# Optimization experiments

Measured on AMD Instinct MI355X. Metric: run time of the kernel, lower is better.

The kernel has to match this reference:

```python
import jax, jax.numpy as jnp
import numpy as np

N_EMBD = 384
HEAD_SIZE = 64
BLOCK_SIZE = 64
SCALE = HEAD_SIZE * N_EMBD ** (-0.5)  # non-standard scale from source: k.shape[-1] * C**-0.5


def setup_inputs() -> dict:
    key = jax.random.key(0)
    kx, kk, kq, kv = jax.random.split(key, 4)
    B, T = 2048, BLOCK_SIZE
    x = jax.random.normal(kx, (B, T, N_EMBD), dtype=jnp.float32)
    # torch Linear(n_embd, head_size, bias=False): weight shape [head_size, n_embd], y = x @ W.T
    s = N_EMBD ** -0.5
    Wk = jax.random.uniform(kk, (HEAD_SIZE, N_EMBD), jnp.float32, -s, s)
    Wq = jax.random.uniform(kq, (HEAD_SIZE, N_EMBD), jnp.float32, -s, s)
    Wv = jax.random.uniform(kv, (HEAD_SIZE, N_EMBD), jnp.float32, -s, s)
    return {"x": x, "Wk": Wk, "Wq": Wq, "Wv": Wv}


def reference(x, Wk, Wq, Wv) -> jnp.ndarray:
    B, T, C = x.shape
    k = jnp.einsum("btc,hc->bth", x, Wk)  # [B,T,H]
    q = jnp.einsum("btc,hc->bth", x, Wq)
    v = jnp.einsum("btc,hc->bth", x, Wv)
    wei = jnp.einsum("bth,bsh->bts", q, k) * SCALE  # [B,T,T]
    causal = jnp.tril(jnp.ones((T, T), dtype=bool))
    wei = jnp.where(causal, wei, -jnp.inf)
    wei = jax.nn.softmax(wei, axis=-1)
    out = jnp.einsum("bts,bsh->bth", wei, v)  # [B,T,H]
    return out
```

## Files before the change

### kernel.cpp

```cpp
#include <hip/hip_runtime.h>

typedef _Float16 f16;
typedef _Float16 f16x8 __attribute__((ext_vector_type(8)));
typedef _Float16 f16x4 __attribute__((ext_vector_type(4)));
typedef float    f32x4 __attribute__((ext_vector_type(4)));

#define MFMA16(a, b, c) __builtin_amdgcn_mfma_f32_16x16x32_f16((a), (b), (c), 0, 0, 0)

constexpr int T = 64;
constexpr int C = 384;
constexpr int H = 64;
constexpr float SCALE = 3.26598632371090f;

__device__ __forceinline__ void load_lds16(const float* g, float* l) {
  __builtin_amdgcn_global_load_lds(
      (const __attribute__((address_space(1))) void*)g,
      (__attribute__((address_space(3))) void*)l, 16, 0, 0);
}

__global__ void pack_w(const float* __restrict__ Wk, const float* __restrict__ Wq,
                       const float* __restrict__ Wv, f16* __restrict__ Wp) {
  int tid = blockIdx.x * blockDim.x + threadIdx.x;
  if (tid >= 3 * 12 * 4 * 64) return;
  int lane = tid & 63;
  int tile = tid >> 6;
  int ht = tile & 3;
  int kt = (tile >> 2) % 12;
  int wi = tile / 48;
  const float* W = (wi == 0) ? Wk : ((wi == 1) ? Wq : Wv);
  int h = 16 * ht + (lane & 15);
  int c = 32 * kt + 8 * (lane >> 4);
  const float* src = W + h * C + c;
  f16x8 v;
#pragma unroll
  for (int j = 0; j < 8; ++j) v[j] = (f16)src[j];
  int tile2 = kt * 12 + wi * 4 + ht;
  *(f16x8*)(Wp + (size_t)tile2 * 512 + lane * 8) = v;
}

__global__ __launch_bounds__(256, 4) void proj_kqv(
    const float* __restrict__ x, const f16* __restrict__ Wp,
    f16* __restrict__ kg, f16* __restrict__ qg, f16* __restrict__ vtg) {
  __shared__ float xc[2][2048];

  const int b = blockIdx.x;
  const int tid = threadIdx.x;
  const int w = tid >> 6;
  const int lane = tid & 63;
  const int l15 = lane & 15;
  const int g = lane >> 4;

  const f32x4 vzero = {0.0f, 0.0f, 0.0f, 0.0f};
  f32x4 acc[3][4];
#pragma unroll
  for (int c = 0; c < 3; ++c)
#pragma unroll
    for (int tt = 0; tt < 4; ++tt) acc[c][tt] = vzero;

  const f16* wp_base[3];
  bool isV[3];
#pragma unroll
  for (int c = 0; c < 3; ++c) {
    int combo = 3 * w + c;
    wp_base[c] = Wp + (size_t)combo * 512 + lane * 8;
    isV[c] = (combo >= 8);
  }

  const float* xbase = x + (size_t)b * T * C;
  const float* gsrc = xbase + (size_t)(16 * w + l15) * C + g * 8;

  load_lds16(gsrc + 0, &xc[0][(2 * w + 0) * 256]);
  load_lds16(gsrc + 4, &xc[0][(2 * w + 1) * 256]);
  f16x8 wpc[3], wpn[3];
#pragma unroll
  for (int c = 0; c < 3; ++c) wpc[c] = *(const f16x8*)(wp_base[c]);
  asm volatile("s_waitcnt vmcnt(0)" ::: "memory");
  __builtin_amdgcn_s_barrier();

#pragma unroll
  for (int kt = 0; kt < 12; ++kt) {
    const int cur = kt & 1;
    if (kt + 1 < 12) {
      load_lds16(gsrc + (kt + 1) * 32 + 0, &xc[cur ^ 1][(2 * w + 0) * 256]);
      load_lds16(gsrc + (kt + 1) * 32 + 4, &xc[cur ^ 1][(2 * w + 1) * 256]);
#pragma unroll
      for (int c = 0; c < 3; ++c)
        wpn[c] = *(const f16x8*)(wp_base[c] + (size_t)(kt + 1) * 6144);
    }

    f16x8 xf[4];
#pragma unroll
    for (int tt = 0; tt < 4; ++tt) {
      f32x4 A0 = *(const f32x4*)&xc[cur][(2 * tt + 0) * 256 + lane * 4];
      f32x4 A1 = *(const f32x4*)&xc[cur][(2 * tt + 1) * 256 + lane * 4];
#pragma unroll
      for (int j = 0; j < 4; ++j) { xf[tt][j] = (f16)A0[j]; xf[tt][4 + j] = (f16)A1[j]; }
    }
#pragma unroll
    for (int c = 0; c < 3; ++c) {
      f16x8 wf = wpc[c];
      if (!isV[c]) {
#pragma unroll
        for (int tt = 0; tt < 4; ++tt) acc[c][tt] = MFMA16(wf, xf[tt], acc[c][tt]);
      } else {
#pragma unroll
        for (int tt = 0; tt < 4; ++tt) acc[c][tt] = MFMA16(xf[tt], wf, acc[c][tt]);
      }
      wpc[c] = wpn[c];
    }
    asm volatile("s_waitcnt vmcnt(0)" ::: "memory");
    __builtin_amdgcn_s_barrier();
  }

  f16* vt_lds = (f16*)&xc[0][0];
#pragma unroll
  for (int c = 0; c < 3; ++c) {
    int combo = 3 * w + c;
    int m = combo >> 2;
    int ht = combo & 3;
#pragma unroll
    for (int tt = 0; tt < 4; ++tt) {
      f16x4 pd;
#pragma unroll
      for (int r = 0; r < 4; ++r) pd[r] = (f16)acc[c][tt][r];
      if (m == 0) {
        *(f16x4*)(kg + ((size_t)b * 64 + 16 * tt + l15) * 64 + 16 * ht + 4 * g) = pd;
      } else if (m == 1) {
        *(f16x4*)(qg + ((size_t)b * 64 + 16 * tt + l15) * 64 + 16 * ht + 4 * g) = pd;
      } else {
        *(f16x4*)&vt_lds[(16 * ht + l15) * 68 + 16 * tt + 4 * g] = pd;
      }
    }
  }
  __syncthreads();
#pragma unroll
  for (int r = 0; r < 2; ++r) {
    int idx = tid + r * 256;
    f16x8 vv = *(const f16x8*)&vt_lds[(idx >> 3) * 68 + (idx & 7) * 8];
    *(f16x8*)(vtg + (size_t)b * 4096 + idx * 8) = vv;
  }
}

__global__ __launch_bounds__(256, 5) void attn64(
    const f16* __restrict__ kg, const f16* __restrict__ qg,
    const f16* __restrict__ vtg, float* __restrict__ out) {
  __shared__ f16 qp_lds[64][72];
  __shared__ f16 k_lds[64][72];
  __shared__ f16 vT_lds[64][72];

  const int b = blockIdx.x;
  const int tid = threadIdx.x;
  const int w = tid >> 6;
  const int lane = tid & 63;
  const int l15 = lane & 15;
  const int g = lane >> 4;
  const int t_ = 16 * w + l15;

  const size_t tb = (size_t)b * 4096;
  const int i0 = tid, i1 = tid + 256;
  f16x8 ka = *(const f16x8*)(kg + tb + (size_t)i0 * 8);
  f16x8 kb = *(const f16x8*)(kg + tb + (size_t)i1 * 8);
  f16x8 qa = *(const f16x8*)(qg + tb + (size_t)i0 * 8);
  f16x8 qb = *(const f16x8*)(qg + tb + (size_t)i1 * 8);
  f16x8 va = *(const f16x8*)(vtg + tb + (size_t)i0 * 8);
  f16x8 vb = *(const f16x8*)(vtg + tb + (size_t)i1 * 8);
  *(f16x8*)&k_lds[i0 >> 3][(i0 & 7) * 8] = ka;
  *(f16x8*)&k_lds[i1 >> 3][(i1 & 7) * 8] = kb;
  *(f16x8*)&qp_lds[i0 >> 3][(i0 & 7) * 8] = qa;
  *(f16x8*)&qp_lds[i1 >> 3][(i1 & 7) * 8] = qb;
  *(f16x8*)&vT_lds[i0 >> 3][(i0 & 7) * 8] = va;
  *(f16x8*)&vT_lds[i1 >> 3][(i1 & 7) * 8] = vb;
  __syncthreads();

  const f32x4 vzero = {0.0f, 0.0f, 0.0f, 0.0f};

  f32x4 accs[4];
#pragma unroll
  for (int i = 0; i < 4; ++i) accs[i] = vzero;
#pragma unroll
  for (int kt = 0; kt < 2; ++kt) {
    f16x8 qf = *(const f16x8*)&qp_lds[t_][32 * kt + 8 * g];
#pragma unroll
    for (int mt = 0; mt < 4; ++mt) {
      f16x8 kf = *(const f16x8*)&k_lds[16 * mt + l15][32 * kt + 8 * g];
      accs[mt] = MFMA16(kf, qf, accs[mt]);
    }
  }

  float e[16];
  float mx = -__builtin_inff();
#pragma unroll
  for (int mt = 0; mt < 4; ++mt) {
#pragma unroll
    for (int r = 0; r < 4; ++r) {
      int s = 16 * mt + 4 * g + r;
      float lv = accs[mt][r] * SCALE;
      lv = (s <= t_) ? lv : -__builtin_inff();
      e[mt * 4 + r] = lv;
      mx = fmaxf(mx, lv);
    }
  }
  mx = fmaxf(mx, __shfl_xor(mx, 16));
  mx = fmaxf(mx, __shfl_xor(mx, 32));
  float sm = 0.0f;
#pragma unroll
  for (int i = 0; i < 16; ++i) { e[i] = __expf(e[i] - mx); sm += e[i]; }
  sm += __shfl_xor(sm, 16);
  sm += __shfl_xor(sm, 32);
  const float inv = 1.0f / sm;
#pragma unroll
  for (int mt = 0; mt < 4; ++mt) {
    f16x4 pp;
#pragma unroll
    for (int r = 0; r < 4; ++r) pp[r] = (f16)(e[mt * 4 + r] * inv);
    *(f16x4*)&qp_lds[t_][16 * mt + 4 * g] = pp;
  }

  f32x4 acco[4];
#pragma unroll
  for (int i = 0; i < 4; ++i) acco[i] = vzero;
#pragma unroll
  for (int kt = 0; kt < 2; ++kt) {
    f16x8 pf = *(const f16x8*)&qp_lds[t_][32 * kt + 8 * g];
#pragma unroll
    for (int mt = 0; mt < 4; ++mt) {
      f16x8 vf = *(const f16x8*)&vT_lds[16 * mt + l15][32 * kt + 8 * g];
      acco[mt] = MFMA16(vf, pf, acco[mt]);
    }
  }

  float* orow = out + ((size_t)b * T + t_) * H;
#pragma unroll
  for (int mt = 0; mt < 4; ++mt) {
    *(f32x4*)(orow + 16 * mt + 4 * g) = acco[mt];
  }
}

extern "C" void kernel_launch(void* const* d_in, const int* in_sizes, int n_in,
                              void* d_out, int out_size, void* d_ws, size_t ws_size,
                              hipStream_t stream) {
  const float* x  = (const float*)d_in[0];
  const float* Wk = (const float*)d_in[1];
  const float* Wq = (const float*)d_in[2];
  const float* Wv = (const float*)d_in[3];
  float* out = (float*)d_out;

  f16* Wp  = (f16*)d_ws;
  f16* kg  = (f16*)((char*)d_ws + (1 << 18));
  f16* qg  = kg + (size_t)2048 * 64 * 64;
  f16* vtg = qg + (size_t)2048 * 64 * 64;

  pack_w<<<36, 256, 0, stream>>>(Wk, Wq, Wv, Wp);
  proj_kqv<<<2048, 256, 0, stream>>>(x, Wp, kg, qg, vtg);
  attn64<<<2048, 256, 0, stream>>>(kg, qg, vtg, out);
}
```

Measured before the change: 354.4 us.

## Restructure projection so each wave owns a row tile and streams x through registers

Each wave now computes all 12 output column blocks (K, Q, V) for its own 16 rows of x, so the x tile can be loaded straight into registers with a 4-deep prefetch ring. This drops the LDS staging and the per-k-step barriers. In exchange, every wave loads all 12 weight fragments per k step, which raises L2/global weight traffic and register pressure. Launch bounds are lowered to 2 blocks per SIMD to make room for the extra registers.

```diff
diff --git a/kernel.cpp b/kernel.cpp
--- a/kernel.cpp
+++ b/kernel.cpp
@@ -11,12 +11,6 @@
 constexpr int C = 384;
 constexpr int H = 64;
 constexpr float SCALE = 3.26598632371090f;
-
-__device__ __forceinline__ void load_lds16(const float* g, float* l) {
-  __builtin_amdgcn_global_load_lds(
-      (const __attribute__((address_space(1))) void*)g,
-      (__attribute__((address_space(3))) void*)l, 16, 0, 0);
-}
 
 __global__ void pack_w(const float* __restrict__ Wk, const float* __restrict__ Wq,
                        const float* __restrict__ Wv, f16* __restrict__ Wp) {
@@ -38,10 +32,10 @@
   *(f16x8*)(Wp + (size_t)tile2 * 512 + lane * 8) = v;
 }
 
-__global__ __launch_bounds__(256, 4) void proj_kqv(
+__global__ __launch_bounds__(256, 2) void proj_reg(
     const float* __restrict__ x, const f16* __restrict__ Wp,
     f16* __restrict__ kg, f16* __restrict__ qg, f16* __restrict__ vtg) {
-  __shared__ float xc[2][2048];
+  __shared__ f16 vt_lds[64][68];
 
   const int b = blockIdx.x;
   const int tid = threadIdx.x;
@@ -51,92 +45,78 @@
   const int g = lane >> 4;
 
   const f32x4 vzero = {0.0f, 0.0f, 0.0f, 0.0f};
-  f32x4 acc[3][4];
-#pragma unroll
-  for (int c = 0; c < 3; ++c)
-#pragma unroll
-    for (int tt = 0; tt < 4; ++tt) acc[c][tt] = vzero;
-
-  const f16* wp_base[3];
-  bool isV[3];
-#pragma unroll
-  for (int c = 0; c < 3; ++c) {
-    int combo = 3 * w + c;
-    wp_base[c] = Wp + (size_t)combo * 512 + lane * 8;
-    isV[c] = (combo >= 8);
-  }
-
-  const float* xbase = x + (size_t)b * T * C;
-  const float* gsrc = xbase + (size_t)(16 * w + l15) * C + g * 8;
-
-  load_lds16(gsrc + 0, &xc[0][(2 * w + 0) * 256]);
-  load_lds16(gsrc + 4, &xc[0][(2 * w + 1) * 256]);
-  f16x8 wpc[3], wpn[3];
-#pragma unroll
-  for (int c = 0; c < 3; ++c) wpc[c] = *(const f16x8*)(wp_base[c]);
-  asm volatile("s_waitcnt vmcnt(0)" ::: "memory");
-  __builtin_amdgcn_s_barrier();
+  f32x4 acc[12];
+#pragma unroll
+  for (int cb = 0; cb < 12; ++cb) acc[cb] = vzero;
+
+  const float* gsrc = x + (size_t)b * T * C + (size_t)(16 * w + l15) * C + 8 * g;
+  const f16* wsrc = Wp + lane * 8;
+
+  f32x4 xa[4], xb[4];
+#pragma unroll
+  for (int i = 0; i < 4; ++i) {
+    xa[i] = *(const f32x4*)(gsrc + i * 32 + 0);
+    xb[i] = *(const f32x4*)(gsrc + i * 32 + 4);
+  }
+  f16x8 wpc[12], wpn[12];
+#pragma unroll
+  for (int cb = 0; cb < 12; ++cb)
+    wpc[cb] = *(const f16x8*)(wsrc + (size_t)cb * 512);
 
 #pragma unroll
   for (int kt = 0; kt < 12; ++kt) {
-    const int cur = kt & 1;
+    const int sl = kt & 3;
+    f16x8 xf;
+    {
+      f32x4 A0 = xa[sl], A1 = xb[sl];
+#pragma unroll
+      for (int j = 0; j < 4; ++j) { xf[j] = (f16)A0[j]; xf[4 + j] = (f16)A1[j]; }
+    }
+    if (kt + 4 < 12) {
+      xa[sl] = *(const f32x4*)(gsrc + (kt + 4) * 32 + 0);
+      xb[sl] = *(const f32x4*)(gsrc + (kt + 4) * 32 + 4);
+    }
     if (kt + 1 < 12) {
-      load_lds16(gsrc + (kt + 1) * 32 + 0, &xc[cur ^ 1][(2 * w + 0) * 256]);
-      load_lds16(gsrc + (kt + 1) * 32 + 4, &xc[cur ^ 1][(2 * w + 1) * 256]);
-#pragma unroll
-      for (int c = 0; c < 3; ++c)
-        wpn[c] = *(const f16x8*)(wp_base[c] + (size_t)(kt + 1) * 6144);
-    }
-
-    f16x8 xf[4];
-#pragma unroll
-    for (int tt = 0; tt < 4; ++tt) {
-      f32x4 A0 = *(const f32x4*)&xc[cur][(2 * tt + 0) * 256 + lane * 4];
-      f32x4 A1 = *(const f32x4*)&xc[cur][(2 * tt + 1) * 256 + lane * 4];
-#pragma unroll
-      for (int j = 0; j < 4; ++j) { xf[tt][j] = (f16)A0[j]; xf[tt][4 + j] = (f16)A1[j]; }
-    }
-#pragma unroll
-    for (int c = 0; c < 3; ++c) {
-      f16x8 wf = wpc[c];
-      if (!isV[c]) {
-#pragma unroll
-        for (int tt = 0; tt < 4; ++tt) acc[c][tt] = MFMA16(wf, xf[tt], acc[c][tt]);
-      } else {
-#pragma unroll
-        for (int tt = 0; tt < 4; ++tt) acc[c][tt] = MFMA16(xf[tt], wf, acc[c][tt]);
-      }
-      wpc[c] = wpn[c];
-    }
-    asm volatile("s_waitcnt vmcnt(0)" ::: "memory");
-    __builtin_amdgcn_s_barrier();
-  }
-
-  f16* vt_lds = (f16*)&xc[0][0];
-#pragma unroll
-  for (int c = 0; c < 3; ++c) {
-    int combo = 3 * w + c;
-    int m = combo >> 2;
-    int ht = combo & 3;
-#pragma unroll
-    for (int tt = 0; tt < 4; ++tt) {
-      f16x4 pd;
-#pragma unroll
-      for (int r = 0; r < 4; ++r) pd[r] = (f16)acc[c][tt][r];
-      if (m == 0) {
-        *(f16x4*)(kg + ((size_t)b * 64 + 16 * tt + l15) * 64 + 16 * ht + 4 * g) = pd;
-      } else if (m == 1) {
-        *(f16x4*)(qg + ((size_t)b * 64 + 16 * tt + l15) * 64 + 16 * ht + 4 * g) = pd;
-      } else {
-        *(f16x4*)&vt_lds[(16 * ht + l15) * 68 + 16 * tt + 4 * g] = pd;
-      }
-    }
+#pragma unroll
+      for (int cb = 0; cb < 12; ++cb)
+        wpn[cb] = *(const f16x8*)(wsrc + ((size_t)(kt + 1) * 12 + cb) * 512);
+    }
+#pragma unroll
+    for (int cb = 0; cb < 8; ++cb)
+      acc[cb] = MFMA16(wpc[cb], xf, acc[cb]);
+#pragma unroll
+    for (int cb = 8; cb < 12; ++cb)
+      acc[cb] = MFMA16(xf, wpc[cb], acc[cb]);
+#pragma unroll
+    for (int cb = 0; cb < 12; ++cb) wpc[cb] = wpn[cb];
+  }
+
+#pragma unroll
+  for (int ht = 0; ht < 4; ++ht) {
+    f16x4 pd;
+#pragma unroll
+    for (int r = 0; r < 4; ++r) pd[r] = (f16)acc[0 + ht][r];
+    *(f16x4*)(kg + ((size_t)b * 64 + 16 * w + l15) * 64 + 16 * ht + 4 * g) = pd;
+  }
+#pragma unroll
+  for (int ht = 0; ht < 4; ++ht) {
+    f16x4 pd;
+#pragma unroll
+    for (int r = 0; r < 4; ++r) pd[r] = (f16)acc[4 + ht][r];
+    *(f16x4*)(qg + ((size_t)b * 64 + 16 * w + l15) * 64 + 16 * ht + 4 * g) = pd;
+  }
+#pragma unroll
+  for (int ht = 0; ht < 4; ++ht) {
+    f16x4 pd;
+#pragma unroll
+    for (int r = 0; r < 4; ++r) pd[r] = (f16)acc[8 + ht][r];
+    *(f16x4*)&vt_lds[16 * ht + l15][16 * w + 4 * g] = pd;
   }
   __syncthreads();
 #pragma unroll
   for (int r = 0; r < 2; ++r) {
     int idx = tid + r * 256;
-    f16x8 vv = *(const f16x8*)&vt_lds[(idx >> 3) * 68 + (idx & 7) * 8];
+    f16x8 vv = *(const f16x8*)&vt_lds[idx >> 3][(idx & 7) * 8];
     *(f16x8*)(vtg + (size_t)b * 4096 + idx * 8) = vv;
   }
 }
@@ -251,6 +231,6 @@
   f16* vtg = qg + (size_t)2048 * 64 * 64;
 
   pack_w<<<36, 256, 0, stream>>>(Wk, Wq, Wv, Wp);
-  proj_kqv<<<2048, 256, 0, stream>>>(x, Wp, kg, qg, vtg);
+  proj_reg<<<2048, 256, 0, stream>>>(x, Wp, kg, qg, vtg);
   attn64<<<2048, 256, 0, stream>>>(kg, qg, vtg, out);
 }
```

Result: no change. 356.9 us (+0.7%).
